# Kernel tuning notes

Hardware: AMD Instinct MI355X
Metric: run time of the kernel (lower is better)

## Reference

```python
import jax, jax.numpy as jnp
import numpy as np

D_MODEL = 512
B, T = 4, 4096


def setup_inputs() -> dict:
    key = jax.random.key(0)
    ks = jax.random.split(key, 5)
    s = 1.0 / np.sqrt(D_MODEL)  # roughly Linear init scale
    return {
        "x": jax.random.normal(ks[0], (B, T, D_MODEL), dtype=jnp.float32),
        "W_q": jax.random.normal(ks[1], (D_MODEL, D_MODEL), dtype=jnp.float32) * s,
        "W_k": jax.random.normal(ks[2], (D_MODEL, D_MODEL), dtype=jnp.float32) * s,
        "W_v": jax.random.normal(ks[3], (D_MODEL, D_MODEL), dtype=jnp.float32) * s,
        "W_o": jax.random.normal(ks[4], (D_MODEL, D_MODEL), dtype=jnp.float32) * s,
    }


def reference(x, W_q, W_k, W_v, W_o):
    # torch nn.Linear(bias=False): y = x @ W.T
    q = jnp.einsum('btd,ed->bte', x, W_q)
    k = jnp.einsum('btd,ed->bte', x, W_k)
    v = jnp.einsum('btd,ed->bte', x, W_v)
    Tq, Tk = q.shape[1], k.shape[1]
    scale = 1.0 / jnp.sqrt(jnp.float32(x.shape[-1]))
    scores = jnp.einsum('bqd,bkd->bqk', q, k) * scale  # [B,T,T]
    causal = jnp.tril(jnp.ones((Tq, Tk), dtype=bool))  # mask triu(diag=1) -> keep lower triangle
    scores = jnp.where(causal[None, :, :], scores, -jnp.inf)
    attn = jax.nn.softmax(scores, axis=-1)
    ctx = jnp.einsum('bqk,bkd->bqd', attn, v)
    out = jnp.einsum('btd,ed->bte', ctx, W_o)
    return out
```

## Files before the change

### kernel.cpp

```cpp
#include <hip/hip_runtime.h>
#include <hip/hip_bf16.h>
#include <math.h>

#define D 512
#define BB 4
#define TT 4096
#define KT 32

typedef __attribute__((ext_vector_type(8))) short short8v;
typedef __attribute__((ext_vector_type(4))) short short4v;
typedef __attribute__((ext_vector_type(4))) float float4v;

__device__ inline short f2bf(float x) {
    __hip_bfloat16 h = __float2bfloat16(x);
    return *reinterpret_cast<short*>(&h);
}
__device__ inline float bf2f(short s) {
    __hip_bfloat16 h = *reinterpret_cast<__hip_bfloat16*>(&s);
    return __bfloat162float(h);
}

__global__ __launch_bounds__(256) void gemm_qkv(
    const float* __restrict__ x,
    const float* __restrict__ Wq, const float* __restrict__ Wk, const float* __restrict__ Wv,
    __hip_bfloat16* __restrict__ q, __hip_bfloat16* __restrict__ k, __hip_bfloat16* __restrict__ v)
{
    const float* W; __hip_bfloat16* C; float alpha;
    if (blockIdx.z == 0)      { W = Wq; C = q; alpha = 0.044194173824159216f; }
    else if (blockIdx.z == 1) { W = Wk; C = k; alpha = 1.f; }
    else                      { W = Wv; C = v; alpha = 1.f; }

    __shared__ short As[64][72];
    __shared__ short Bs[64][72];
    const int tid = threadIdx.x;
    const int m0 = blockIdx.x * 64, n0 = blockIdx.y * 64;
    const int w = tid >> 6, lane = tid & 63, lm = lane & 15, g = lane >> 4;

    float4v acc[4];
    #pragma unroll
    for (int i = 0; i < 4; ++i) acc[i] = (float4v){0.f,0.f,0.f,0.f};

    for (int k0 = 0; k0 < 512; k0 += 64) {
        __syncthreads();
        #pragma unroll
        for (int u = 0; u < 4; ++u) {
            int ch = tid + 256*u;
            int r = ch >> 4, c = (ch & 15) * 4;
            float4 xv = *reinterpret_cast<const float4*>(x + (size_t)(m0 + r)*512 + k0 + c);
            short4v sv = { f2bf(xv.x), f2bf(xv.y), f2bf(xv.z), f2bf(xv.w) };
            *reinterpret_cast<short4v*>(&As[r][c]) = sv;
        }
        #pragma unroll
        for (int u = 0; u < 4; ++u) {
            int ch = tid + 256*u;
            int r = ch >> 4, c = (ch & 15) * 4;
            float4 wv = *reinterpret_cast<const float4*>(W + (size_t)(n0 + r)*512 + k0 + c);
            short4v sv = { f2bf(wv.x), f2bf(wv.y), f2bf(wv.z), f2bf(wv.w) };
            *reinterpret_cast<short4v*>(&Bs[r][c]) = sv;
        }
        __syncthreads();
        #pragma unroll
        for (int ks = 0; ks < 2; ++ks) {
            short8v a = *reinterpret_cast<const short8v*>(&As[16*w + lm][ks*32 + 8*g]);
            #pragma unroll
            for (int nt = 0; nt < 4; ++nt) {
                short8v bv = *reinterpret_cast<const short8v*>(&Bs[16*nt + lm][ks*32 + 8*g]);
                acc[nt] = __builtin_amdgcn_mfma_f32_16x16x32_bf16(a, bv, acc[nt], 0, 0, 0);
            }
        }
    }
    #pragma unroll
    for (int nt = 0; nt < 4; ++nt)
        #pragma unroll
        for (int r = 0; r < 4; ++r) {
            int row = m0 + 16*w + 4*g + r;
            int col = n0 + 16*nt + lm;
            C[(size_t)row*512 + col] = __float2bfloat16(acc[nt][r] * alpha);
        }
}

__global__ __launch_bounds__(256) void transpose_v(
    const __hip_bfloat16* __restrict__ vin, __hip_bfloat16* __restrict__ vout)
{
    const int tid = threadIdx.x;
    const int b = blockIdx.y;
    const int t = blockIdx.x * 32 + (tid & 31);
    const int tau = t & 31;
    const int tp = (t & ~31) + 8*((tau & 15) >> 2) + (tau & 3) + 4*(tau >> 4);
    const short* src = (const short*)vin + (size_t)(b*TT + t)*D;
    short* dst = (short*)vout + (size_t)b*D*TT;
    #pragma unroll
    for (int u = 0; u < 8; ++u) {
        int cf = (tid >> 5) + 8*u;
        short8v vv = *reinterpret_cast<const short8v*>(src + cf*8);
        #pragma unroll
        for (int i = 0; i < 8; ++i)
            dst[(size_t)(cf*8 + i)*TT + tp] = vv[i];
    }
}

__global__ __launch_bounds__(512, 1) void attn_split(
    const __hip_bfloat16* __restrict__ qg, const __hip_bfloat16* __restrict__ kg,
    const __hip_bfloat16* __restrict__ vtg,
    __hip_bfloat16* __restrict__ U0, __hip_bfloat16* __restrict__ U1,
    __hip_bfloat16* __restrict__ U2, __hip_bfloat16* __restrict__ U3,
    float* __restrict__ mArr, float* __restrict__ lArr)
{
    __shared__ short Ks[2][KT][512];
    __shared__ short Vs[2][512][32];

    const int tid = threadIdx.x;
    const int w = tid >> 6, lane = tid & 63, lm = lane & 15, g = lane >> 4;
    const int qgp = w;
    const int idx = blockIdx.x;
    const int b  = idx & 3;
    const int u  = idx >> 2;
    const int pr = u >> 2;
    const int s  = u & 3;

    const short* qp = (const short*)qg  + (size_t)b*TT*D;
    const short* kp = (const short*)kg  + (size_t)b*TT*D;
    const short* vp = (const short*)vtg + (size_t)b*D*TT;

    short* Uo = (short*)((s == 0) ? U0 : (s == 1) ? U1 : (s == 2) ? U2 : U3);
    float* mo = mArr + (size_t)s * BB * TT;
    float* lo = lArr + (size_t)s * BB * TT;

    const int vswz = (lane & 3) ^ ((lane >> 3) & 3);

    const short* k0p = &Ks[0][lm][g*8];
    const short* k1p = &Ks[1][lm][g*8];
    const int vcid = g ^ ((lm >> 1) & 3);
    const short* v0p = &Vs[0][lm][vcid*8];
    const short* v1p = &Vs[1][lm][vcid*8];

    #define STAGE_KV(T, BUF) do {                                                  \
        const short* kt_ = kp + (size_t)(T) * KT * D;                              \
        const int ksv_ = (T) * KT;                                                 \
        _Pragma("unroll")                                                          \
        for (int i_ = 0; i_ < 4; ++i_) {                                           \
            int r_ = 4*w + i_;                                                     \
            int c_ = (lane ^ ((r_ & 15) << 2)) & 63;                               \
            __builtin_amdgcn_global_load_lds(                                      \
                (const __attribute__((address_space(1))) void*)(kt_ + (size_t)r_*D + c_*8), \
                (__attribute__((address_space(3))) void*)(&Ks[BUF][r_][0]),        \
                16, 0, 0);                                                         \
        }                                                                          \
        _Pragma("unroll")                                                          \
        for (int i_ = 0; i_ < 4; ++i_) {                                           \
            int d0_ = 64*w + 16*i_;                                                \
            int row_ = d0_ + (lane >> 2);                                          \
            __builtin_amdgcn_global_load_lds(                                      \
                (const __attribute__((address_space(1))) void*)(vp + (size_t)row_*TT + ksv_ + vswz*8), \
                (__attribute__((address_space(3))) void*)(&Vs[BUF][d0_][0]),       \
                16, 0, 0);                                                         \
        }                                                                          \
    } while (0)

    #pragma unroll 1
    for (int phase = 0; phase < 2; ++phase) {
        const int qb = phase ? (31 - pr) : pr;
        const int qbase = qb * 128;
        const int qrow  = qbase + 16*qgp + lm;
        const int t0  = s * (qb + 1);
        const int cnt = qb + 1;

        short8v qf[16];
        #pragma unroll
        for (int ss = 0; ss < 16; ++ss)
            qf[ss] = *reinterpret_cast<const short8v*>(qp + (size_t)qrow*D + 32*ss + 8*g);

        float4v acc[32];
        #pragma unroll
        for (int i = 0; i < 32; ++i) acc[i] = (float4v){0.f,0.f,0.f,0.f};
        float m_r = -INFINITY, l_par = 0.f;

        __syncthreads();
        STAGE_KV(t0, 0);

        for (int i = 0; i < cnt; ++i) {
            const int t = t0 + i;
            const int ks0 = t * KT;
            __syncthreads();
            if (i + 1 < cnt) STAGE_KV(t + 1, (i + 1) & 1);

            const short* kc = (i & 1) ? k1p : k0p;
            const short* vc = (i & 1) ? v1p : v0p;

            float4v s0a = (float4v){0.f,0.f,0.f,0.f}, s0b = (float4v){0.f,0.f,0.f,0.f};
            float4v s1a = (float4v){0.f,0.f,0.f,0.f}, s1b = (float4v){0.f,0.f,0.f,0.f};
            #pragma unroll
            for (int ss = 0; ss < 16; ++ss) {
                int off = (ss ^ lm) << 5;
                short8v a0 = *reinterpret_cast<const short8v*>(kc + off);
                short8v a1 = *reinterpret_cast<const short8v*>(kc + off + 8192);
                if (ss & 1) {
                    s0b = __builtin_amdgcn_mfma_f32_16x16x32_bf16(a0, qf[ss], s0b, 0, 0, 0);
                    s1b = __builtin_amdgcn_mfma_f32_16x16x32_bf16(a1, qf[ss], s1b, 0, 0, 0);
                } else {
                    s0a = __builtin_amdgcn_mfma_f32_16x16x32_bf16(a0, qf[ss], s0a, 0, 0, 0);
                    s1a = __builtin_amdgcn_mfma_f32_16x16x32_bf16(a1, qf[ss], s1a, 0, 0, 0);
                }
            }
            float4v s0, s1;
            #pragma unroll
            for (int r = 0; r < 4; ++r) { s0[r] = s0a[r] + s0b[r]; s1[r] = s1a[r] + s1b[r]; }

            float p[8];
            #pragma unroll
            for (int r = 0; r < 4; ++r) {
                int kj0 = ks0 + 4*g + r;
                p[r]     = (kj0      <= qrow) ? s0[r] : -3.0e38f;
                p[r + 4] = (kj0 + 16 <= qrow) ? s1[r] : -3.0e38f;
            }
            float mx = p[0];
            #pragma unroll
            for (int i2 = 1; i2 < 8; ++i2) mx = fmaxf(mx, p[i2]);

            if (!__all(mx <= m_r + 8.f)) {
                float mrow = fmaxf(mx, __shfl_xor(mx, 16));
                mrow = fmaxf(mrow, __shfl_xor(mrow, 32));
                mrow = fmaxf(mrow, m_r);
                float corr = __expf(m_r - mrow);
                m_r = mrow;
                l_par *= corr;
                #pragma unroll
                for (int dt = 0; dt < 32; ++dt) {
                    acc[dt][0] *= corr; acc[dt][1] *= corr;
                    acc[dt][2] *= corr; acc[dt][3] *= corr;
                }
            }
            #pragma unroll
            for (int i2 = 0; i2 < 8; ++i2) {
                float e = __expf(p[i2] - m_r);
                p[i2] = (p[i2] > -1.0e37f) ? e : 0.f;
                l_par += p[i2];
            }

            short8v pf;
            #pragma unroll
            for (int i2 = 0; i2 < 8; ++i2) pf[i2] = f2bf(p[i2]);

            #pragma unroll
            for (int dt = 0; dt < 32; ++dt) {
                short8v vf = *reinterpret_cast<const short8v*>(vc + dt*512);
                acc[dt] = __builtin_amdgcn_mfma_f32_16x16x32_bf16(vf, pf, acc[dt], 0, 0, 0);
            }
        }

        float l = l_par + __shfl_xor(l_par, 16);
        l += __shfl_xor(l, 32);
        const int orow = qbase + 16*qgp + lm;
        short* up = Uo + (size_t)(b*TT + orow)*D;
        #pragma unroll
        for (int dt = 0; dt < 32; ++dt) {
            short4v o = { f2bf(acc[dt][0]), f2bf(acc[dt][1]),
                          f2bf(acc[dt][2]), f2bf(acc[dt][3]) };
            *reinterpret_cast<short4v*>(up + 16*dt + 4*g) = o;
        }
        if (g == 0) {
            mo[(size_t)b*TT + orow] = m_r;
            lo[(size_t)b*TT + orow] = l;
        }
    }
    #undef STAGE_KV
}

__global__ __launch_bounds__(256) void merge_quads(
    const __hip_bfloat16* __restrict__ U0, const __hip_bfloat16* __restrict__ U1,
    const __hip_bfloat16* __restrict__ U2, const __hip_bfloat16* __restrict__ U3,
    const float* __restrict__ mArr, const float* __restrict__ lArr,
    __hip_bfloat16* __restrict__ ctx)
{
    const int BT = BB * TT;
    const int gidx = blockIdx.x * 256 + threadIdx.x;
    const int row = gidx >> 6;
    const int c = (gidx & 63) * 8;
    float m0 = mArr[row], m1 = mArr[BT + row], m2 = mArr[2*BT + row], m3 = mArr[3*BT + row];
    float ms = fmaxf(fmaxf(m0, m1), fmaxf(m2, m3));
    float w0 = __expf(m0 - ms), w1 = __expf(m1 - ms);
    float w2 = __expf(m2 - ms), w3 = __expf(m3 - ms);
    float l = lArr[row]*w0 + lArr[BT + row]*w1 + lArr[2*BT + row]*w2 + lArr[3*BT + row]*w3;
    float inv = 1.f / l;
    w0 *= inv; w1 *= inv; w2 *= inv; w3 *= inv;
    size_t off = (size_t)row * D + c;
    short8v a = *reinterpret_cast<const short8v*>((const short*)U0 + off);
    short8v b = *reinterpret_cast<const short8v*>((const short*)U1 + off);
    short8v d = *reinterpret_cast<const short8v*>((const short*)U2 + off);
    short8v e = *reinterpret_cast<const short8v*>((const short*)U3 + off);
    short8v o;
    #pragma unroll
    for (int i = 0; i < 8; ++i)
        o[i] = f2bf(bf2f(a[i])*w0 + bf2f(b[i])*w1 + bf2f(d[i])*w2 + bf2f(e[i])*w3);
    *reinterpret_cast<short8v*>((short*)ctx + off) = o;
}

__global__ __launch_bounds__(256) void gemm_out(
    const __hip_bfloat16* __restrict__ Ab, const float* __restrict__ W,
    float* __restrict__ Cf)
{
    __shared__ short As[64][72];
    __shared__ short Bs[64][72];
    const int tid = threadIdx.x;
    const int m0 = blockIdx.x * 64, n0 = blockIdx.y * 64;
    const int w = tid >> 6, lane = tid & 63, lm = lane & 15, g = lane >> 4;
    const short* Ap = (const short*)Ab;

    float4v acc[4];
    #pragma unroll
    for (int i = 0; i < 4; ++i) acc[i] = (float4v){0.f,0.f,0.f,0.f};

    for (int k0 = 0; k0 < 512; k0 += 64) {
        __syncthreads();
        #pragma unroll
        for (int u = 0; u < 2; ++u) {
            int ch = tid + 256*u;
            int r = ch >> 3, c = (ch & 7) * 8;
            *reinterpret_cast<short8v*>(&As[r][c]) =
                *reinterpret_cast<const short8v*>(Ap + (size_t)(m0 + r)*512 + k0 + c);
        }
        #pragma unroll
        for (int u = 0; u < 4; ++u) {
            int ch = tid + 256*u;
            int r = ch >> 4, c = (ch & 15) * 4;
            float4 wv = *reinterpret_cast<const float4*>(W + (size_t)(n0 + r)*512 + k0 + c);
            short4v sv = { f2bf(wv.x), f2bf(wv.y), f2bf(wv.z), f2bf(wv.w) };
            *reinterpret_cast<short4v*>(&Bs[r][c]) = sv;
        }
        __syncthreads();
        #pragma unroll
        for (int ks = 0; ks < 2; ++ks) {
            short8v a = *reinterpret_cast<const short8v*>(&As[16*w + lm][ks*32 + 8*g]);
            #pragma unroll
            for (int nt = 0; nt < 4; ++nt) {
                short8v bv = *reinterpret_cast<const short8v*>(&Bs[16*nt + lm][ks*32 + 8*g]);
                acc[nt] = __builtin_amdgcn_mfma_f32_16x16x32_bf16(a, bv, acc[nt], 0, 0, 0);
            }
        }
    }
    #pragma unroll
    for (int nt = 0; nt < 4; ++nt)
        #pragma unroll
        for (int r = 0; r < 4; ++r) {
            int row = m0 + 16*w + 4*g + r;
            int col = n0 + 16*nt + lm;
            Cf[(size_t)row*512 + col] = acc[nt][r];
        }
}

extern "C" void kernel_launch(void* const* d_in, const int* in_sizes, int n_in,
                              void* d_out, int out_size, void* d_ws, size_t ws_size,
                              hipStream_t stream) {
    const float* x  = (const float*)d_in[0];
    const float* Wq = (const float*)d_in[1];
    const float* Wk = (const float*)d_in[2];
    const float* Wv = (const float*)d_in[3];
    const float* Wo = (const float*)d_in[4];
    float* out = (float*)d_out;

    const size_t n = (size_t)BB * TT * D;
    __hip_bfloat16* qb_  = (__hip_bfloat16*)d_ws;
    __hip_bfloat16* kb_  = qb_ + n;
    __hip_bfloat16* vb_  = kb_ + n;
    __hip_bfloat16* vt_  = vb_ + n;
    __hip_bfloat16* ctxb = vt_ + n;
    __hip_bfloat16* U1   = ctxb + n;
    __hip_bfloat16* U2   = U1 + n;
    __hip_bfloat16* U3   = U2 + n;
    float* mArr = (float*)(U3 + n);
    float* lArr = mArr + (size_t)4 * BB * TT;
    __hip_bfloat16* U0 = (__hip_bfloat16*)out;

    gemm_qkv<<<dim3(256, 8, 3), 256, 0, stream>>>(x, Wq, Wk, Wv, qb_, kb_, vb_);
    transpose_v<<<dim3(TT / 32, BB), 256, 0, stream>>>(vb_, vt_);
    attn_split<<<dim3(64 * BB), 512, 0, stream>>>(qb_, kb_, vt_, U0, U1, U2, U3, mArr, lArr);
    merge_quads<<<dim3(BB * TT / 4), 256, 0, stream>>>(U0, U1, U2, U3, mArr, lArr, ctxb);
    gemm_out<<<dim3(256, 8, 1), 256, 0, stream>>>(ctxb, Wo, out);
}
```

Before: 259.6 us.

## Fuse Q/K/V projections per block to reuse x tile, add MFMA priority hints

The QKV GEMM now computes all three projections in one block, loading and converting each x tile to bf16 once instead of three times, and cuts the grid from 3x to 1x blocks. Each block holds three weight tiles in LDS and three times as many accumulators, which raises register and LDS use and may lower occupancy. The attention kernel also wraps its QK and PV MFMA loops in s_setprio to favour matrix-issuing waves.

```diff
diff --git a/kernel.cpp b/kernel.cpp
--- a/kernel.cpp
+++ b/kernel.cpp
@@ -25,20 +25,17 @@
     const float* __restrict__ Wq, const float* __restrict__ Wk, const float* __restrict__ Wv,
     __hip_bfloat16* __restrict__ q, __hip_bfloat16* __restrict__ k, __hip_bfloat16* __restrict__ v)
 {
-    const float* W; __hip_bfloat16* C; float alpha;
-    if (blockIdx.z == 0)      { W = Wq; C = q; alpha = 0.044194173824159216f; }
-    else if (blockIdx.z == 1) { W = Wk; C = k; alpha = 1.f; }
-    else                      { W = Wv; C = v; alpha = 1.f; }
-
     __shared__ short As[64][72];
-    __shared__ short Bs[64][72];
+    __shared__ short Bs[3][64][72];
     const int tid = threadIdx.x;
     const int m0 = blockIdx.x * 64, n0 = blockIdx.y * 64;
     const int w = tid >> 6, lane = tid & 63, lm = lane & 15, g = lane >> 4;
 
-    float4v acc[4];
-    #pragma unroll
-    for (int i = 0; i < 4; ++i) acc[i] = (float4v){0.f,0.f,0.f,0.f};
+    float4v acc[3][4];
+    #pragma unroll
+    for (int z = 0; z < 3; ++z)
+        #pragma unroll
+        for (int i = 0; i < 4; ++i) acc[z][i] = (float4v){0.f,0.f,0.f,0.f};
 
     for (int k0 = 0; k0 < 512; k0 += 64) {
         __syncthreads();
@@ -51,32 +48,43 @@
             *reinterpret_cast<short4v*>(&As[r][c]) = sv;
         }
         #pragma unroll
-        for (int u = 0; u < 4; ++u) {
-            int ch = tid + 256*u;
-            int r = ch >> 4, c = (ch & 15) * 4;
-            float4 wv = *reinterpret_cast<const float4*>(W + (size_t)(n0 + r)*512 + k0 + c);
-            short4v sv = { f2bf(wv.x), f2bf(wv.y), f2bf(wv.z), f2bf(wv.w) };
-            *reinterpret_cast<short4v*>(&Bs[r][c]) = sv;
+        for (int z = 0; z < 3; ++z) {
+            const float* W = (z == 0) ? Wq : (z == 1) ? Wk : Wv;
+            #pragma unroll
+            for (int u = 0; u < 4; ++u) {
+                int ch = tid + 256*u;
+                int r = ch >> 4, c = (ch & 15) * 4;
+                float4 wv = *reinterpret_cast<const float4*>(W + (size_t)(n0 + r)*512 + k0 + c);
+                short4v sv = { f2bf(wv.x), f2bf(wv.y), f2bf(wv.z), f2bf(wv.w) };
+                *reinterpret_cast<short4v*>(&Bs[z][r][c]) = sv;
+            }
         }
         __syncthreads();
         #pragma unroll
         for (int ks = 0; ks < 2; ++ks) {
             short8v a = *reinterpret_cast<const short8v*>(&As[16*w + lm][ks*32 + 8*g]);
             #pragma unroll
-            for (int nt = 0; nt < 4; ++nt) {
-                short8v bv = *reinterpret_cast<const short8v*>(&Bs[16*nt + lm][ks*32 + 8*g]);
-                acc[nt] = __builtin_amdgcn_mfma_f32_16x16x32_bf16(a, bv, acc[nt], 0, 0, 0);
-            }
-        }
-    }
-    #pragma unroll
-    for (int nt = 0; nt < 4; ++nt)
-        #pragma unroll
-        for (int r = 0; r < 4; ++r) {
-            int row = m0 + 16*w + 4*g + r;
-            int col = n0 + 16*nt + lm;
-            C[(size_t)row*512 + col] = __float2bfloat16(acc[nt][r] * alpha);
-        }
+            for (int z = 0; z < 3; ++z)
+                #pragma unroll
+                for (int nt = 0; nt < 4; ++nt) {
+                    short8v bv = *reinterpret_cast<const short8v*>(&Bs[z][16*nt + lm][ks*32 + 8*g]);
+                    acc[z][nt] = __builtin_amdgcn_mfma_f32_16x16x32_bf16(a, bv, acc[z][nt], 0, 0, 0);
+                }
+        }
+    }
+    #pragma unroll
+    for (int z = 0; z < 3; ++z) {
+        __hip_bfloat16* C = (z == 0) ? q : (z == 1) ? k : v;
+        const float alpha = (z == 0) ? 0.044194173824159216f : 1.f;
+        #pragma unroll
+        for (int nt = 0; nt < 4; ++nt)
+            #pragma unroll
+            for (int r = 0; r < 4; ++r) {
+                int row = m0 + 16*w + 4*g + r;
+                int col = n0 + 16*nt + lm;
+                C[(size_t)row*512 + col] = __float2bfloat16(acc[z][nt][r] * alpha);
+            }
+    }
 }
 
 __global__ __launch_bounds__(256) void transpose_v(
@@ -189,6 +197,7 @@
 
             float4v s0a = (float4v){0.f,0.f,0.f,0.f}, s0b = (float4v){0.f,0.f,0.f,0.f};
             float4v s1a = (float4v){0.f,0.f,0.f,0.f}, s1b = (float4v){0.f,0.f,0.f,0.f};
+            __builtin_amdgcn_s_setprio(1);
             #pragma unroll
             for (int ss = 0; ss < 16; ++ss) {
                 int off = (ss ^ lm) << 5;
@@ -202,6 +211,7 @@
                     s1a = __builtin_amdgcn_mfma_f32_16x16x32_bf16(a1, qf[ss], s1a, 0, 0, 0);
                 }
             }
+            __builtin_amdgcn_s_setprio(0);
             float4v s0, s1;
             #pragma unroll
             for (int r = 0; r < 4; ++r) { s0[r] = s0a[r] + s0b[r]; s1[r] = s1a[r] + s1b[r]; }
@@ -241,11 +251,13 @@
             #pragma unroll
             for (int i2 = 0; i2 < 8; ++i2) pf[i2] = f2bf(p[i2]);
 
+            __builtin_amdgcn_s_setprio(1);
             #pragma unroll
             for (int dt = 0; dt < 32; ++dt) {
                 short8v vf = *reinterpret_cast<const short8v*>(vc + dt*512);
                 acc[dt] = __builtin_amdgcn_mfma_f32_16x16x32_bf16(vf, pf, acc[dt], 0, 0, 0);
             }
+            __builtin_amdgcn_s_setprio(0);
         }
 
         float l = l_par + __shfl_xor(l_par, 16);
@@ -371,7 +383,7 @@
     float* lArr = mArr + (size_t)4 * BB * TT;
     __hip_bfloat16* U0 = (__hip_bfloat16*)out;
 
-    gemm_qkv<<<dim3(256, 8, 3), 256, 0, stream>>>(x, Wq, Wk, Wv, qb_, kb_, vb_);
+    gemm_qkv<<<dim3(256, 8), 256, 0, stream>>>(x, Wq, Wk, Wv, qb_, kb_, vb_);
     transpose_v<<<dim3(TT / 32, BB), 256, 0, stream>>>(vb_, vt_);
     attn_split<<<dim3(64 * BB), 512, 0, stream>>>(qb_, kb_, vt_, U0, U1, U2, U3, mArr, lArr);
     merge_quads<<<dim3(BB * TT / 4), 256, 0, stream>>>(U0, U1, U2, U3, mArr, lArr, ctxb);
```

Measured after the change: 244.2 us. -5.9%, faster.
